# Optimization experiments

Measured on AMD Instinct MI355X. Metric: run time of the kernel, lower is better.

## Reference

```python
import jax, jax.numpy as jnp
import numpy as np
import math

B, N, D = 4, 16384, 256
M, H = 64, 8
HD = D // H

def setup_inputs() -> dict:
    key = jax.random.key(0)
    ks = jax.random.split(key, 5)
    s = 1.0 / math.sqrt(D)
    return {
        "x": jax.random.normal(ks[0], (B, N, D), dtype=jnp.float32),
        "Ws": jax.random.normal(ks[1], (M, D), dtype=jnp.float32) * s,
        "bs": jnp.zeros((M,), dtype=jnp.float32),
        "Wqkv": jax.random.normal(ks[2], (3 * D, D), dtype=jnp.float32) * s,
        "Wo": jax.random.normal(ks[3], (D, D), dtype=jnp.float32) * s,
        "bo": jnp.zeros((D,), dtype=jnp.float32),
    }

def reference(x, Ws, bs, Wqkv, Wo, bo):
    # slice weights: softmax over N (dim=1), matching the torch code exactly
    logits = jnp.einsum('bnd,md->bnm', x, Ws) + bs          # [B,N,M]
    weights = jax.nn.softmax(logits, axis=1)                # softmax over N
    # pooling: tokens[b,m,d] = sum_n w[b,n,m] * x[b,n,d]
    tokens = jnp.einsum('bnm,bnd->bmd', weights, x)         # [B,M,D]
    # qkv projection (no bias)
    qkv = jnp.einsum('bmd,ed->bme', tokens, Wqkv)           # [B,M,3D]
    qkv = qkv.reshape(B, M, 3, H, HD)
    q = qkv[:, :, 0].transpose(0, 2, 1, 3)                  # [B,H,M,HD]
    k = qkv[:, :, 1].transpose(0, 2, 1, 3)
    v = qkv[:, :, 2].transpose(0, 2, 1, 3)
    scale = 1.0 / math.sqrt(HD)
    attn = jax.nn.softmax(jnp.einsum('bhmd,bhkd->bhmk', q, k) * scale, axis=-1)
    token_out = jnp.einsum('bhmk,bhkd->bhmd', attn, v)      # [B,H,M,HD]
    token_out = token_out.transpose(0, 2, 1, 3).reshape(B, M, D)
    token_out = jnp.einsum('bmd,ed->bme', token_out, Wo) + bo
    # unpooling: out[b,n,d] = sum_m w[b,n,m] * token_out[b,m,d]
    out = jnp.einsum('bnm,bmd->bnd', weights, token_out)    # [B,N,D]
    return out
```

## Files before the change

### kernel.cpp

```cpp
#include <hip/hip_runtime.h>
#include <math.h>

constexpr int B = 4;
constexpr int N = 16384;
constexpr int D = 256;
constexpr int M = 64;
constexpr int H = 8;
constexpr int NSLOT = 128;

typedef __attribute__((ext_vector_type(8))) short short8;
typedef __attribute__((ext_vector_type(4))) float floatx4;

__device__ __forceinline__ float4 ld4(const float* p) {
  return *reinterpret_cast<const float4*>(p);
}
__device__ __forceinline__ unsigned short f2bf(float f) {
  unsigned u = __float_as_uint(f);
  unsigned r = (u + 0x7fffu + ((u >> 16) & 1u)) >> 16;
  return (unsigned short)r;
}

__global__ __launch_bounds__(256) void k0_prep(
    const float* __restrict__ Ws, const float* __restrict__ Wqkv,
    const float* __restrict__ Wo, unsigned short* __restrict__ WsB,
    unsigned short* __restrict__ WqkvB, unsigned short* __restrict__ WoB,
    float* __restrict__ denom, float* __restrict__ tokO) {
  const int g = blockIdx.x * 256 + threadIdx.x;
  if (g < 32768)
    *reinterpret_cast<float2*>(&tokO[g * 2]) = make_float2(0.f, 0.f);
  if (g < 128)
    *reinterpret_cast<float2*>(&denom[g * 2]) = make_float2(0.f, 0.f);
  const float* src;
  unsigned short* dst;
  int off;
  if (g < 2048) {
    src = Ws; dst = WsB; off = g;
  } else if (g < 26624) {
    src = Wqkv; dst = WqkvB; off = g - 2048;
  } else {
    src = Wo; dst = WoB; off = g - 26624;
  }
  const float4 a = ld4(&src[(size_t)off * 8]);
  const float4 c = ld4(&src[(size_t)off * 8 + 4]);
  unsigned d0 = (unsigned)f2bf(a.x) | ((unsigned)f2bf(a.y) << 16);
  unsigned d1 = (unsigned)f2bf(a.z) | ((unsigned)f2bf(a.w) << 16);
  unsigned d2 = (unsigned)f2bf(c.x) | ((unsigned)f2bf(c.y) << 16);
  unsigned d3 = (unsigned)f2bf(c.z) | ((unsigned)f2bf(c.w) << 16);
  *reinterpret_cast<uint4*>(&dst[(size_t)off * 8]) = make_uint4(d0, d1, d2, d3);
}

__global__ __launch_bounds__(256, 2) void k12_fused(
    const float* __restrict__ x, const unsigned short* __restrict__ WsB,
    const float* __restrict__ bs, unsigned short* __restrict__ En,
    float* __restrict__ denom, float* __restrict__ tokensP) {
  __shared__ unsigned short Wt[64][264];
  __shared__ unsigned short EsT[64][70];
  __shared__ unsigned short XsT[256][70];
  __shared__ float red[64];
  const int b = blockIdx.y;
  const int nb0 = blockIdx.x * 128;
  const int tid = threadIdx.x;
  const int w = tid >> 6, l = tid & 63;
  const int l15 = l & 15;
  const int q8 = (l >> 4) * 8;
  const int r4 = (l >> 4) * 4;
  const int ar = w * 16 + l15;

  float4 fx0[16];
  {
    const float* xr = &x[((size_t)(b * N + nb0 + ar)) * D];
#pragma unroll
    for (int ks = 0; ks < 8; ++ks) {
      fx0[2 * ks] = ld4(&xr[ks * 32 + q8]);
      fx0[2 * ks + 1] = ld4(&xr[ks * 32 + q8 + 4]);
    }
  }
#pragma unroll
  for (int p = 0; p < 8; ++p) {
    const int u = p * 256 + tid;
    const int row = u >> 5;
    const int c = (u & 31) * 8;
    *reinterpret_cast<short8*>(&Wt[row][c]) =
        *reinterpret_cast<const short8*>(&WsB[(size_t)row * 256 + c]);
  }
  if (tid < 64) red[tid] = 0.0f;
  __syncthreads();

  floatx4 acc2[16];
#pragma unroll
  for (int i = 0; i < 16; ++i) acc2[i] = {0.f, 0.f, 0.f, 0.f};

  float4 fx1[16];
  short8 afr0[8], afr1[8];
  floatx4 acc[4];

#define K12_CVT(FX, AFR)                                               \
  do {                                                                 \
    _Pragma("unroll") for (int ks = 0; ks < 8; ++ks) {                 \
      const float4 a0 = FX[2 * ks], a1 = FX[2 * ks + 1];               \
      short8 tt;                                                       \
      tt[0] = (short)f2bf(a0.x); tt[1] = (short)f2bf(a0.y);            \
      tt[2] = (short)f2bf(a0.z); tt[3] = (short)f2bf(a0.w);            \
      tt[4] = (short)f2bf(a1.x); tt[5] = (short)f2bf(a1.y);            \
      tt[6] = (short)f2bf(a1.z); tt[7] = (short)f2bf(a1.w);            \
      AFR[ks] = tt;                                                    \
    }                                                                  \
  } while (0)

#define K12_SCATTER(AFR)                                               \
  do {                                                                 \
    _Pragma("unroll") for (int ks = 0; ks < 8; ++ks)                   \
        _Pragma("unroll") for (int j = 0; j < 8; ++j)                  \
            XsT[ks * 32 + q8 + j][ar] = (unsigned short)AFR[ks][j];    \
  } while (0)

#define K12_LOGITS(AFR)                                                \
  do {                                                                 \
    _Pragma("unroll") for (int i = 0; i < 4; ++i)                      \
        acc[i] = {0.f, 0.f, 0.f, 0.f};                                 \
    _Pragma("unroll") for (int ks = 0; ks < 8; ++ks) {                 \
      _Pragma("unroll") for (int mt = 0; mt < 4; ++mt) {               \
        short8 bf =                                                    \
            *reinterpret_cast<short8*>(&Wt[mt * 16 + l15][ks * 32 + q8]); \
        acc[mt] = __builtin_amdgcn_mfma_f32_16x16x32_bf16(AFR[ks], bf, \
                                                          acc[mt], 0, 0, 0); \
      }                                                                \
    }                                                                  \
  } while (0)

#define K12_EPILOG(N0)                                                 \
  do {                                                                 \
    _Pragma("unroll") for (int mt = 0; mt < 4; ++mt) {                 \
      const int m = mt * 16 + l15;                                     \
      const float bsm = bs[m];                                         \
      float s = 0.0f;                                                  \
      _Pragma("unroll") for (int r = 0; r < 4; ++r) {                  \
        const int n = w * 16 + r4 + r;                                 \
        const float e = __expf(acc[mt][r] + bsm);                      \
        s += e;                                                        \
        const unsigned short eb = f2bf(e);                             \
        EsT[m][w * 16 + r4 + r] = eb;                                  \
        En[((size_t)(b * N + (N0) + n)) * M + m] = eb;                 \
      }                                                                \
      atomicAdd(&red[m], s);                                           \
    }                                                                  \
  } while (0)

#define K12_POOL()                                                     \
  do {                                                                 \
    _Pragma("unroll") for (int ks2 = 0; ks2 < 2; ++ks2) {              \
      const int nf = ks2 * 32 + q8;                                    \
      short8 a = *reinterpret_cast<short8*>(&EsT[w * 16 + l15][nf]);   \
      _Pragma("unroll") for (int dt4 = 0; dt4 < 16; ++dt4) {           \
        short8 bf = *reinterpret_cast<short8*>(&XsT[dt4 * 16 + l15][nf]); \
        acc2[dt4] = __builtin_amdgcn_mfma_f32_16x16x32_bf16(a, bf,     \
                                                            acc2[dt4], 0, 0, 0); \
      }                                                                \
    }                                                                  \
  } while (0)

  K12_CVT(fx0, afr0);
  {
    const float* xr = &x[((size_t)(b * N + nb0 + 64 + ar)) * D];
#pragma unroll
    for (int ks = 0; ks < 8; ++ks) {
      fx1[2 * ks] = ld4(&xr[ks * 32 + q8]);
      fx1[2 * ks + 1] = ld4(&xr[ks * 32 + q8 + 4]);
    }
  }
  K12_SCATTER(afr0);
  K12_LOGITS(afr0);
  K12_EPILOG(nb0);
  K12_CVT(fx1, afr1);
  __syncthreads();
  K12_POOL();
  __syncthreads();

  K12_SCATTER(afr1);
  K12_LOGITS(afr1);
  K12_EPILOG(nb0 + 64);
  __syncthreads();
  K12_POOL();

  if (tid < 64) atomicAdd(&denom[b * M + tid], red[tid]);
  float* op = tokensP + ((size_t)(b * NSLOT + blockIdx.x) * M) * D;
#pragma unroll
  for (int dt4 = 0; dt4 < 16; ++dt4)
#pragma unroll
    for (int r = 0; r < 4; ++r)
      op[(w * 16 + r4 + r) * D + dt4 * 16 + l15] = acc2[dt4][r];
#undef K12_CVT
#undef K12_SCATTER
#undef K12_LOGITS
#undef K12_EPILOG
#undef K12_POOL
}

__global__ __launch_bounds__(256) void k2r_reduce(
    const float* __restrict__ tokensP, float* __restrict__ tokens) {
  const int b = blockIdx.x >> 6;
  const int m = blockIdx.x & 63;
  const int d = threadIdx.x;
  const float* base = tokensP + ((size_t)(b * NSLOT) * M + m) * D + d;
  float s0 = 0.f, s1 = 0.f, s2 = 0.f, s3 = 0.f;
#pragma unroll 4
  for (int s = 0; s < NSLOT; s += 4) {
    s0 += base[(size_t)(s + 0) * M * D];
    s1 += base[(size_t)(s + 1) * M * D];
    s2 += base[(size_t)(s + 2) * M * D];
    s3 += base[(size_t)(s + 3) * M * D];
  }
  tokens[((size_t)(b * M) + m) * D + d] = (s0 + s1) + (s2 + s3);
}

__global__ __launch_bounds__(256) void k_fa(
    const float* __restrict__ tokens, const unsigned short* __restrict__ WqkvB,
    const unsigned short* __restrict__ WoB, const float* __restrict__ denom,
    float* __restrict__ tokO) {
  __shared__ __align__(16) char smem[84480];
  unsigned short* const At = reinterpret_cast<unsigned short*>(smem);
  unsigned short* const Wq = reinterpret_cast<unsigned short*>(smem + 33792);
  float* const qt = reinterpret_cast<float*>(smem);
  float* const kt = reinterpret_cast<float*>(smem + 8704);
  float* const vv = reinterpret_cast<float*>(smem + 17408);
  float* const P  = reinterpret_cast<float*>(smem + 26624);
  float* const ao = reinterpret_cast<float*>(smem + 44032);
  const int b = blockIdx.x >> 3;
  const int h = blockIdx.x & 7;
  const int tid = threadIdx.x;
  const int w = tid >> 6, l = tid & 63;
  const int l15 = l & 15;
  const int q8 = (l >> 4) * 8;
  const int r4 = (l >> 4) * 4;

#pragma unroll
  for (int p = 0; p < 16; ++p) {
    const int i = p * 256 + tid;
    const int row = i >> 6;
    const int c4 = (i & 63) * 4;
    float4 av = ld4(&tokens[((size_t)(b * M + row)) * D + c4]);
    unsigned a0 = (unsigned)f2bf(av.x) | ((unsigned)f2bf(av.y) << 16);
    unsigned a1 = (unsigned)f2bf(av.z) | ((unsigned)f2bf(av.w) << 16);
    *reinterpret_cast<uint2*>(&At[row * 264 + c4]) = make_uint2(a0, a1);
  }
#pragma unroll
  for (int p = 0; p < 12; ++p) {
    const int u = p * 256 + tid;
    const int row = u >> 5;
    const int c = (u & 31) * 8;
    const int eg = (row < 32) ? (h * 32 + row)
                 : (row < 64) ? (256 + h * 32 + row - 32)
                              : (512 + h * 32 + row - 64);
    *reinterpret_cast<short8*>(&Wq[row * 264 + c]) =
        *reinterpret_cast<const short8*>(&WqkvB[(size_t)eg * 256 + c]);
  }
  float rcp4[4];
#pragma unroll
  for (int r = 0; r < 4; ++r)
    rcp4[r] = 1.0f / denom[b * M + w * 16 + r4 + r];
  __syncthreads();

  floatx4 acc[6] = {{0.f, 0.f, 0.f, 0.f}, {0.f, 0.f, 0.f, 0.f},
                    {0.f, 0.f, 0.f, 0.f}, {0.f, 0.f, 0.f, 0.f},
                    {0.f, 0.f, 0.f, 0.f}, {0.f, 0.f, 0.f, 0.f}};
  const int arow = w * 16 + l15;
#pragma unroll
  for (int ks = 0; ks < 8; ++ks) {
    short8 a = *reinterpret_cast<short8*>(&At[arow * 264 + ks * 32 + q8]);
#pragma unroll
    for (int et = 0; et < 6; ++et) {
      short8 bf = *reinterpret_cast<short8*>(&Wq[(et * 16 + l15) * 264 + ks * 32 + q8]);
      acc[et] = __builtin_amdgcn_mfma_f32_16x16x32_bf16(a, bf, acc[et], 0, 0, 0);
    }
  }
  short8 wof[4];
#pragma unroll
  for (int dt4 = 0; dt4 < 4; ++dt4)
    wof[dt4] = *reinterpret_cast<const short8*>(
        &WoB[(size_t)(w * 64 + dt4 * 16 + l15) * 256 + h * 32 + q8]);
  __syncthreads();

#pragma unroll
  for (int r = 0; r < 4; ++r) {
    const int m = w * 16 + r4 + r;
    const float rc = rcp4[r];
#pragma unroll
    for (int et = 0; et < 6; ++et) {
      const float val = acc[et][r] * rc;
      const int c = (et & 1) * 16 + l15;
      if (et < 2) qt[c * 68 + m] = val;
      else if (et < 4) kt[c * 68 + m] = val;
      else vv[m * 36 + c] = val;
    }
  }
  __syncthreads();

  {
    const int tm4 = (tid & 15) * 4;
    const int tn4 = (tid >> 4) * 4;
    float sacc[4][4] = {};
    for (int k = 0; k < 32; ++k) {
      float4 a4 = ld4(&qt[k * 68 + tn4]);
      float4 b4 = ld4(&kt[k * 68 + tm4]);
#pragma unroll
      for (int i = 0; i < 4; ++i) {
        const float av = (i == 0) ? a4.x : (i == 1) ? a4.y : (i == 2) ? a4.z : a4.w;
        sacc[i][0] = fmaf(av, b4.x, sacc[i][0]);
        sacc[i][1] = fmaf(av, b4.y, sacc[i][1]);
        sacc[i][2] = fmaf(av, b4.z, sacc[i][2]);
        sacc[i][3] = fmaf(av, b4.w, sacc[i][3]);
      }
    }
    const float scale = 0.17677669529663687f;
#pragma unroll
    for (int i = 0; i < 4; ++i)
      *reinterpret_cast<float4*>(&P[(tn4 + i) * 68 + tm4]) =
          make_float4(sacc[i][0] * scale, sacc[i][1] * scale,
                      sacc[i][2] * scale, sacc[i][3] * scale);
  }
  __syncthreads();
  if (tid < 64) {
    float mx = -1e30f;
    for (int j = 0; j < 64; ++j) mx = fmaxf(mx, P[tid * 68 + j]);
    float s = 0.0f;
    for (int j = 0; j < 64; ++j) {
      const float e = expf(P[tid * 68 + j] - mx);
      P[tid * 68 + j] = e;
      s += e;
    }
    const float r = 1.0f / s;
    for (int j = 0; j < 64; ++j) P[tid * 68 + j] *= r;
  }
  __syncthreads();
  if (tid < 128) {
    const int i0 = (tid >> 3) * 4;
    const int c0 = (tid & 7) * 4;
    float o[4][4] = {};
    for (int j = 0; j < 64; ++j) {
      float4 v4 = ld4(&vv[j * 36 + c0]);
#pragma unroll
      for (int ii = 0; ii < 4; ++ii) {
        const float p = P[(i0 + ii) * 68 + j];
        o[ii][0] = fmaf(p, v4.x, o[ii][0]);
        o[ii][1] = fmaf(p, v4.y, o[ii][1]);
        o[ii][2] = fmaf(p, v4.z, o[ii][2]);
        o[ii][3] = fmaf(p, v4.w, o[ii][3]);
      }
    }
#pragma unroll
    for (int ii = 0; ii < 4; ++ii)
#pragma unroll
      for (int jj = 0; jj < 4; ++jj) ao[(i0 + ii) * 36 + c0 + jj] = o[ii][jj];
  }
  __syncthreads();

  floatx4 acc2[4][4] = {{{0.f, 0.f, 0.f, 0.f}, {0.f, 0.f, 0.f, 0.f},
                         {0.f, 0.f, 0.f, 0.f}, {0.f, 0.f, 0.f, 0.f}},
                        {{0.f, 0.f, 0.f, 0.f}, {0.f, 0.f, 0.f, 0.f},
                         {0.f, 0.f, 0.f, 0.f}, {0.f, 0.f, 0.f, 0.f}},
                        {{0.f, 0.f, 0.f, 0.f}, {0.f, 0.f, 0.f, 0.f},
                         {0.f, 0.f, 0.f, 0.f}, {0.f, 0.f, 0.f, 0.f}},
                        {{0.f, 0.f, 0.f, 0.f}, {0.f, 0.f, 0.f, 0.f},
                         {0.f, 0.f, 0.f, 0.f}, {0.f, 0.f, 0.f, 0.f}}};
#pragma unroll
  for (int mt = 0; mt < 4; ++mt) {
    short8 af;
#pragma unroll
    for (int j = 0; j < 8; ++j)
      af[j] = (short)f2bf(ao[(mt * 16 + l15) * 36 + q8 + j]);
#pragma unroll
    for (int dt4 = 0; dt4 < 4; ++dt4)
      acc2[mt][dt4] =
          __builtin_amdgcn_mfma_f32_16x16x32_bf16(af, wof[dt4], acc2[mt][dt4], 0, 0, 0);
  }
#pragma unroll
  for (int mt = 0; mt < 4; ++mt)
#pragma unroll
    for (int dt4 = 0; dt4 < 4; ++dt4)
#pragma unroll
      for (int r = 0; r < 4; ++r) {
        const int m = mt * 16 + r4 + r;
        const int d = w * 64 + dt4 * 16 + l15;
        atomicAdd(&tokO[((size_t)(b * M + m)) * D + d], acc2[mt][dt4][r]);
      }
}

__global__ __launch_bounds__(512, 4) void k6_unpool(
    const unsigned short* __restrict__ En, const float* __restrict__ tokO,
    const float* __restrict__ denom, const float* __restrict__ bo,
    float* __restrict__ out) {
  __shared__ unsigned short EnS[128][72];
  __shared__ unsigned short TpS[64][72];
  const int dt = blockIdx.x, nt = blockIdx.y, b = blockIdx.z;
  const int n0 = nt * 128, d0 = dt * 64;
  const int tid = threadIdx.x;
  const int w = tid >> 6, l = tid & 63;
  const int l15 = l & 15;
  const int q8 = (l >> 4) * 8;
#pragma unroll
  for (int p = 0; p < 2; ++p) {
    const int g = p * 512 + tid;
    const int row = g >> 3;
    const int c8 = (g & 7) * 8;
    *reinterpret_cast<short8*>(&EnS[row][c8]) =
        *reinterpret_cast<const short8*>(
            &En[((size_t)(b * N + n0 + row)) * M + c8]);
  }
  {
    const int m = tid >> 3;
    const int c8 = (tid & 7) * 8;
    const float rc = 1.0f / denom[b * M + m];
    const float* tp = &tokO[((size_t)(b * M + m)) * D + d0 + c8];
    float4 v0 = ld4(tp);
    float4 v1 = ld4(tp + 4);
    float4 bb0 = ld4(&bo[d0 + c8]);
    float4 bb1 = ld4(&bo[d0 + c8 + 4]);
    TpS[c8 + 0][m] = f2bf((v0.x + bb0.x) * rc);
    TpS[c8 + 1][m] = f2bf((v0.y + bb0.y) * rc);
    TpS[c8 + 2][m] = f2bf((v0.z + bb0.z) * rc);
    TpS[c8 + 3][m] = f2bf((v0.w + bb0.w) * rc);
    TpS[c8 + 4][m] = f2bf((v1.x + bb1.x) * rc);
    TpS[c8 + 5][m] = f2bf((v1.y + bb1.y) * rc);
    TpS[c8 + 6][m] = f2bf((v1.z + bb1.z) * rc);
    TpS[c8 + 7][m] = f2bf((v1.w + bb1.w) * rc);
  }
  __syncthreads();
  floatx4 acc[4] = {{0.f, 0.f, 0.f, 0.f},
                    {0.f, 0.f, 0.f, 0.f},
                    {0.f, 0.f, 0.f, 0.f},
                    {0.f, 0.f, 0.f, 0.f}};
  const int arow = w * 16 + l15;
#pragma unroll
  for (int ks = 0; ks < 2; ++ks) {
    short8 a = *reinterpret_cast<short8*>(&EnS[arow][ks * 32 + q8]);
#pragma unroll
    for (int dtile = 0; dtile < 4; ++dtile) {
      short8 bf = *reinterpret_cast<short8*>(
          &TpS[dtile * 16 + l15][ks * 32 + q8]);
      acc[dtile] =
          __builtin_amdgcn_mfma_f32_16x16x32_bf16(a, bf, acc[dtile], 0, 0, 0);
    }
  }
#pragma unroll
  for (int dtile = 0; dtile < 4; ++dtile)
#pragma unroll
    for (int r = 0; r < 4; ++r) {
      const int n = n0 + w * 16 + (l >> 4) * 4 + r;
      const int d = d0 + dtile * 16 + l15;
      out[((size_t)(b * N + n)) * D + d] = acc[dtile][r];
    }
}

extern "C" void kernel_launch(void* const* d_in, const int* in_sizes, int n_in,
                              void* d_out, int out_size, void* d_ws,
                              size_t ws_size, hipStream_t stream) {
  const float* x = (const float*)d_in[0];
  const float* Ws = (const float*)d_in[1];
  const float* bs = (const float*)d_in[2];
  const float* Wqkv = (const float*)d_in[3];
  const float* Wo = (const float*)d_in[4];
  const float* bo = (const float*)d_in[5];
  float* out = (float*)d_out;

  char* p = (char*)d_ws;
  unsigned short* En = (unsigned short*)p;    p += (size_t)B * N * M * 2;
  float* denom = (float*)p;                   p += (size_t)B * M * 4;
  float* tokens = (float*)p;                  p += (size_t)B * M * D * 4;
  float* tokO = (float*)p;                    p += (size_t)B * M * D * 4;
  float* tokensP = (float*)p;                 p += (size_t)B * NSLOT * M * D * 4;
  unsigned short* WsB = (unsigned short*)p;   p += (size_t)M * D * 2;
  unsigned short* WqkvB = (unsigned short*)p; p += (size_t)3 * D * D * 2;
  unsigned short* WoB = (unsigned short*)p;   p += (size_t)D * D * 2;

  k0_prep<<<dim3(136), 256, 0, stream>>>(Ws, Wqkv, Wo, WsB, WqkvB, WoB,
                                         denom, tokO);
  k12_fused<<<dim3(N / 128, B), 256, 0, stream>>>(x, WsB, bs, En, denom,
                                                  tokensP);
  k2r_reduce<<<dim3(B * M), 256, 0, stream>>>(tokensP, tokens);
  k_fa<<<dim3(B * H), 256, 0, stream>>>(tokens, WqkvB, WoB, denom, tokO);
  k6_unpool<<<dim3(D / 64, N / 128, B), 512, 0, stream>>>(En, tokO, denom, bo,
                                                          out);
}
```

Measured before the change: 168.6 us.

## Drop prep kernel, convert weights inline, reduce denominators deterministically, widen unpool tiles

```diff
diff --git a/kernel.cpp b/kernel.cpp
--- a/kernel.cpp
+++ b/kernel.cpp
@@ -19,40 +19,18 @@
   unsigned r = (u + 0x7fffu + ((u >> 16) & 1u)) >> 16;
   return (unsigned short)r;
 }
-
-__global__ __launch_bounds__(256) void k0_prep(
-    const float* __restrict__ Ws, const float* __restrict__ Wqkv,
-    const float* __restrict__ Wo, unsigned short* __restrict__ WsB,
-    unsigned short* __restrict__ WqkvB, unsigned short* __restrict__ WoB,
-    float* __restrict__ denom, float* __restrict__ tokO) {
-  const int g = blockIdx.x * 256 + threadIdx.x;
-  if (g < 32768)
-    *reinterpret_cast<float2*>(&tokO[g * 2]) = make_float2(0.f, 0.f);
-  if (g < 128)
-    *reinterpret_cast<float2*>(&denom[g * 2]) = make_float2(0.f, 0.f);
-  const float* src;
-  unsigned short* dst;
-  int off;
-  if (g < 2048) {
-    src = Ws; dst = WsB; off = g;
-  } else if (g < 26624) {
-    src = Wqkv; dst = WqkvB; off = g - 2048;
-  } else {
-    src = Wo; dst = WoB; off = g - 26624;
-  }
-  const float4 a = ld4(&src[(size_t)off * 8]);
-  const float4 c = ld4(&src[(size_t)off * 8 + 4]);
+__device__ __forceinline__ uint2 pack8(float4 a, float4 b, unsigned* hi) {
   unsigned d0 = (unsigned)f2bf(a.x) | ((unsigned)f2bf(a.y) << 16);
   unsigned d1 = (unsigned)f2bf(a.z) | ((unsigned)f2bf(a.w) << 16);
-  unsigned d2 = (unsigned)f2bf(c.x) | ((unsigned)f2bf(c.y) << 16);
-  unsigned d3 = (unsigned)f2bf(c.z) | ((unsigned)f2bf(c.w) << 16);
-  *reinterpret_cast<uint4*>(&dst[(size_t)off * 8]) = make_uint4(d0, d1, d2, d3);
+  hi[0] = (unsigned)f2bf(b.x) | ((unsigned)f2bf(b.y) << 16);
+  hi[1] = (unsigned)f2bf(b.z) | ((unsigned)f2bf(b.w) << 16);
+  return make_uint2(d0, d1);
 }
 
 __global__ __launch_bounds__(256, 2) void k12_fused(
-    const float* __restrict__ x, const unsigned short* __restrict__ WsB,
+    const float* __restrict__ x, const float* __restrict__ Ws,
     const float* __restrict__ bs, unsigned short* __restrict__ En,
-    float* __restrict__ denom, float* __restrict__ tokensP) {
+    float* __restrict__ denomP, float* __restrict__ tokensP) {
   __shared__ unsigned short Wt[64][264];
   __shared__ unsigned short EsT[64][70];
   __shared__ unsigned short XsT[256][70];
@@ -76,12 +54,17 @@
     }
   }
 #pragma unroll
-  for (int p = 0; p < 8; ++p) {
-    const int u = p * 256 + tid;
-    const int row = u >> 5;
-    const int c = (u & 31) * 8;
-    *reinterpret_cast<short8*>(&Wt[row][c]) =
-        *reinterpret_cast<const short8*>(&WsB[(size_t)row * 256 + c]);
+  for (int p = 0; p < 4; ++p) {
+    const int i = p * 256 + tid;
+    const int row = i >> 4;
+    const int c16 = (i & 15) * 16;
+    const float* wp = &Ws[(size_t)row * 256 + c16];
+    float4 v0 = ld4(wp), v1 = ld4(wp + 4), v2 = ld4(wp + 8), v3 = ld4(wp + 12);
+    unsigned hi[2];
+    uint2 lo = pack8(v0, v1, hi);
+    *reinterpret_cast<uint4*>(&Wt[row][c16]) = make_uint4(lo.x, lo.y, hi[0], hi[1]);
+    lo = pack8(v2, v3, hi);
+    *reinterpret_cast<uint4*>(&Wt[row][c16 + 8]) = make_uint4(lo.x, lo.y, hi[0], hi[1]);
   }
   if (tid < 64) red[tid] = 0.0f;
   __syncthreads();
@@ -182,7 +165,8 @@
   __syncthreads();
   K12_POOL();
 
-  if (tid < 64) atomicAdd(&denom[b * M + tid], red[tid]);
+  if (tid < 64)
+    denomP[((size_t)(b * NSLOT) + blockIdx.x) * M + tid] = red[tid];
   float* op = tokensP + ((size_t)(b * NSLOT + blockIdx.x) * M) * D;
 #pragma unroll
   for (int dt4 = 0; dt4 < 16; ++dt4)
@@ -197,10 +181,13 @@
 }
 
 __global__ __launch_bounds__(256) void k2r_reduce(
-    const float* __restrict__ tokensP, float* __restrict__ tokens) {
+    const float* __restrict__ tokensP, const float* __restrict__ denomP,
+    unsigned short* __restrict__ tokensB, float* __restrict__ rdenom,
+    float* __restrict__ tokO) {
   const int b = blockIdx.x >> 6;
   const int m = blockIdx.x & 63;
   const int d = threadIdx.x;
+  tokO[(size_t)blockIdx.x * 256 + d] = 0.0f;
   const float* base = tokensP + ((size_t)(b * NSLOT) * M + m) * D + d;
   float s0 = 0.f, s1 = 0.f, s2 = 0.f, s3 = 0.f;
 #pragma unroll 4
@@ -210,12 +197,19 @@
     s2 += base[(size_t)(s + 2) * M * D];
     s3 += base[(size_t)(s + 3) * M * D];
   }
-  tokens[((size_t)(b * M) + m) * D + d] = (s0 + s1) + (s2 + s3);
+  tokensB[((size_t)(b * M) + m) * D + d] = f2bf((s0 + s1) + (s2 + s3));
+  if (d < 64) {
+    float v = denomP[((size_t)(b * NSLOT) + d) * M + m] +
+              denomP[((size_t)(b * NSLOT) + 64 + d) * M + m];
+#pragma unroll
+    for (int off = 32; off > 0; off >>= 1) v += __shfl_down(v, off);
+    if (d == 0) rdenom[b * M + m] = 1.0f / v;
+  }
 }
 
 __global__ __launch_bounds__(256) void k_fa(
-    const float* __restrict__ tokens, const unsigned short* __restrict__ WqkvB,
-    const unsigned short* __restrict__ WoB, const float* __restrict__ denom,
+    const unsigned short* __restrict__ tokensB, const float* __restrict__ Wqkv,
+    const float* __restrict__ Wo, const float* __restrict__ rdenom,
     float* __restrict__ tokO) {
   __shared__ __align__(16) char smem[84480];
   unsigned short* const At = reinterpret_cast<unsigned short*>(smem);
@@ -234,30 +228,35 @@
   const int r4 = (l >> 4) * 4;
 
 #pragma unroll
-  for (int p = 0; p < 16; ++p) {
-    const int i = p * 256 + tid;
-    const int row = i >> 6;
-    const int c4 = (i & 63) * 4;
-    float4 av = ld4(&tokens[((size_t)(b * M + row)) * D + c4]);
-    unsigned a0 = (unsigned)f2bf(av.x) | ((unsigned)f2bf(av.y) << 16);
-    unsigned a1 = (unsigned)f2bf(av.z) | ((unsigned)f2bf(av.w) << 16);
-    *reinterpret_cast<uint2*>(&At[row * 264 + c4]) = make_uint2(a0, a1);
-  }
-#pragma unroll
-  for (int p = 0; p < 12; ++p) {
+  for (int p = 0; p < 8; ++p) {
     const int u = p * 256 + tid;
     const int row = u >> 5;
     const int c = (u & 31) * 8;
+    *reinterpret_cast<short8*>(&At[row * 264 + c]) =
+        *reinterpret_cast<const short8*>(&tokensB[((size_t)(b * M + row)) * 256 + c]);
+  }
+#pragma unroll
+  for (int p = 0; p < 6; ++p) {
+    const int u = p * 256 + tid;
+    const int row = u >> 4;
+    const int c16 = (u & 15) * 16;
     const int eg = (row < 32) ? (h * 32 + row)
                  : (row < 64) ? (256 + h * 32 + row - 32)
                               : (512 + h * 32 + row - 64);
-    *reinterpret_cast<short8*>(&Wq[row * 264 + c]) =
-        *reinterpret_cast<const short8*>(&WqkvB[(size_t)eg * 256 + c]);
+    const float* wp = &Wqkv[(size_t)eg * 256 + c16];
+    float4 v0 = ld4(wp), v1 = ld4(wp + 4), v2 = ld4(wp + 8), v3 = ld4(wp + 12);
+    unsigned hi[2];
+    uint2 lo = pack8(v0, v1, hi);
+    *reinterpret_cast<uint4*>(&Wq[row * 264 + c16]) =
+        make_uint4(lo.x, lo.y, hi[0], hi[1]);
+    lo = pack8(v2, v3, hi);
+    *reinterpret_cast<uint4*>(&Wq[row * 264 + c16 + 8]) =
+        make_uint4(lo.x, lo.y, hi[0], hi[1]);
   }
   float rcp4[4];
 #pragma unroll
   for (int r = 0; r < 4; ++r)
-    rcp4[r] = 1.0f / denom[b * M + w * 16 + r4 + r];
+    rcp4[r] = rdenom[b * M + w * 16 + r4 + r];
   __syncthreads();
 
   floatx4 acc[6] = {{0.f, 0.f, 0.f, 0.f}, {0.f, 0.f, 0.f, 0.f},
@@ -275,9 +274,16 @@
   }
   short8 wof[4];
 #pragma unroll
-  for (int dt4 = 0; dt4 < 4; ++dt4)
-    wof[dt4] = *reinterpret_cast<const short8*>(
-        &WoB[(size_t)(w * 64 + dt4 * 16 + l15) * 256 + h * 32 + q8]);
+  for (int dt4 = 0; dt4 < 4; ++dt4) {
+    const float* wp = &Wo[(size_t)(w * 64 + dt4 * 16 + l15) * 256 + h * 32 + q8];
+    float4 v0 = ld4(wp), v1 = ld4(wp + 4);
+    short8 tt;
+    tt[0] = (short)f2bf(v0.x); tt[1] = (short)f2bf(v0.y);
+    tt[2] = (short)f2bf(v0.z); tt[3] = (short)f2bf(v0.w);
+    tt[4] = (short)f2bf(v1.x); tt[5] = (short)f2bf(v1.y);
+    tt[6] = (short)f2bf(v1.z); tt[7] = (short)f2bf(v1.w);
+    wof[dt4] = tt;
+  }
   __syncthreads();
 
 #pragma unroll
@@ -387,18 +393,18 @@
 
 __global__ __launch_bounds__(512, 4) void k6_unpool(
     const unsigned short* __restrict__ En, const float* __restrict__ tokO,
-    const float* __restrict__ denom, const float* __restrict__ bo,
+    const float* __restrict__ rdenom, const float* __restrict__ bo,
     float* __restrict__ out) {
-  __shared__ unsigned short EnS[128][72];
+  __shared__ unsigned short EnS[256][72];
   __shared__ unsigned short TpS[64][72];
   const int dt = blockIdx.x, nt = blockIdx.y, b = blockIdx.z;
-  const int n0 = nt * 128, d0 = dt * 64;
+  const int n0 = nt * 256, d0 = dt * 64;
   const int tid = threadIdx.x;
   const int w = tid >> 6, l = tid & 63;
   const int l15 = l & 15;
   const int q8 = (l >> 4) * 8;
 #pragma unroll
-  for (int p = 0; p < 2; ++p) {
+  for (int p = 0; p < 4; ++p) {
     const int g = p * 512 + tid;
     const int row = g >> 3;
     const int c8 = (g & 7) * 8;
@@ -409,7 +415,7 @@
   {
     const int m = tid >> 3;
     const int c8 = (tid & 7) * 8;
-    const float rc = 1.0f / denom[b * M + m];
+    const float rc = rdenom[b * M + m];
     const float* tp = &tokO[((size_t)(b * M + m)) * D + d0 + c8];
     float4 v0 = ld4(tp);
     float4 v1 = ld4(tp + 4);
@@ -425,30 +431,33 @@
     TpS[c8 + 7][m] = f2bf((v1.w + bb1.w) * rc);
   }
   __syncthreads();
-  floatx4 acc[4] = {{0.f, 0.f, 0.f, 0.f},
-                    {0.f, 0.f, 0.f, 0.f},
-                    {0.f, 0.f, 0.f, 0.f},
-                    {0.f, 0.f, 0.f, 0.f}};
-  const int arow = w * 16 + l15;
-#pragma unroll
-  for (int ks = 0; ks < 2; ++ks) {
-    short8 a = *reinterpret_cast<short8*>(&EnS[arow][ks * 32 + q8]);
-#pragma unroll
-    for (int dtile = 0; dtile < 4; ++dtile) {
-      short8 bf = *reinterpret_cast<short8*>(
-          &TpS[dtile * 16 + l15][ks * 32 + q8]);
-      acc[dtile] =
-          __builtin_amdgcn_mfma_f32_16x16x32_bf16(a, bf, acc[dtile], 0, 0, 0);
-    }
-  }
-#pragma unroll
-  for (int dtile = 0; dtile < 4; ++dtile)
-#pragma unroll
-    for (int r = 0; r < 4; ++r) {
-      const int n = n0 + w * 16 + (l >> 4) * 4 + r;
-      const int d = d0 + dtile * 16 + l15;
-      out[((size_t)(b * N + n)) * D + d] = acc[dtile][r];
-    }
+#pragma unroll
+  for (int pass = 0; pass < 2; ++pass) {
+    const int arow = pass * 128 + w * 16 + l15;
+    floatx4 acc[4] = {{0.f, 0.f, 0.f, 0.f},
+                      {0.f, 0.f, 0.f, 0.f},
+                      {0.f, 0.f, 0.f, 0.f},
+                      {0.f, 0.f, 0.f, 0.f}};
+#pragma unroll
+    for (int ks = 0; ks < 2; ++ks) {
+      short8 a = *reinterpret_cast<short8*>(&EnS[arow][ks * 32 + q8]);
+#pragma unroll
+      for (int dtile = 0; dtile < 4; ++dtile) {
+        short8 bf = *reinterpret_cast<short8*>(
+            &TpS[dtile * 16 + l15][ks * 32 + q8]);
+        acc[dtile] =
+            __builtin_amdgcn_mfma_f32_16x16x32_bf16(a, bf, acc[dtile], 0, 0, 0);
+      }
+    }
+#pragma unroll
+    for (int dtile = 0; dtile < 4; ++dtile)
+#pragma unroll
+      for (int r = 0; r < 4; ++r) {
+        const int n = n0 + pass * 128 + w * 16 + (l >> 4) * 4 + r;
+        const int d = d0 + dtile * 16 + l15;
+        out[((size_t)(b * N + n)) * D + d] = acc[dtile][r];
+      }
+  }
 }
 
 extern "C" void kernel_launch(void* const* d_in, const int* in_sizes, int n_in,
@@ -463,21 +472,18 @@
   float* out = (float*)d_out;
 
   char* p = (char*)d_ws;
-  unsigned short* En = (unsigned short*)p;    p += (size_t)B * N * M * 2;
-  float* denom = (float*)p;                   p += (size_t)B * M * 4;
-  float* tokens = (float*)p;                  p += (size_t)B * M * D * 4;
-  float* tokO = (float*)p;                    p += (size_t)B * M * D * 4;
-  float* tokensP = (float*)p;                 p += (size_t)B * NSLOT * M * D * 4;
-  unsigned short* WsB = (unsigned short*)p;   p += (size_t)M * D * 2;
-  unsigned short* WqkvB = (unsigned short*)p; p += (size_t)3 * D * D * 2;
-  unsigned short* WoB = (unsigned short*)p;   p += (size_t)D * D * 2;
-
-  k0_prep<<<dim3(136), 256, 0, stream>>>(Ws, Wqkv, Wo, WsB, WqkvB, WoB,
-                                         denom, tokO);
-  k12_fused<<<dim3(N / 128, B), 256, 0, stream>>>(x, WsB, bs, En, denom,
+  unsigned short* En = (unsigned short*)p;  p += (size_t)B * N * M * 2;
+  float* tokensP = (float*)p;               p += (size_t)B * NSLOT * M * D * 4;
+  float* denomP = (float*)p;                p += (size_t)B * NSLOT * M * 4;
+  float* rdenom = (float*)p;                p += (size_t)B * M * 4;
+  unsigned short* tokensB = (unsigned short*)p; p += (size_t)B * M * D * 2;
+  float* tokO = (float*)p;                  p += (size_t)B * M * D * 4;
+
+  k12_fused<<<dim3(N / 128, B), 256, 0, stream>>>(x, Ws, bs, En, denomP,
                                                   tokensP);
-  k2r_reduce<<<dim3(B * M), 256, 0, stream>>>(tokensP, tokens);
-  k_fa<<<dim3(B * H), 256, 0, stream>>>(tokens, WqkvB, WoB, denom, tokO);
-  k6_unpool<<<dim3(D / 64, N / 128, B), 512, 0, stream>>>(En, tokO, denom, bo,
+  k2r_reduce<<<dim3(B * M), 256, 0, stream>>>(tokensP, denomP, tokensB,
+                                              rdenom, tokO);
+  k_fa<<<dim3(B * H), 256, 0, stream>>>(tokensB, Wqkv, Wo, rdenom, tokO);
+  k6_unpool<<<dim3(D / 64, N / 256, B), 512, 0, stream>>>(En, tokO, rdenom, bo,
                                                           out);
 }
```

After: 166.9 us. Within noise of the previous version (-1.0%).
